# Performance work log

Measured on AMD Instinct MI355X. Metric: run time of the kernel, lower is better.

Reference implementation:

```python
import jax, jax.numpy as jnp
import numpy as np

B, T, H = 4096, 200, 64
NU, NI, NC = 100000, 1000000, 1000
AU_HID = 36
EPS = 1e-8


def dice(x, alpha):
    # Dice activation: p = sigmoid(batchnorm(x)); out = p*x + (1-p)*alpha*x
    axes = tuple(range(x.ndim - 1))
    m = jnp.mean(x, axis=axes, keepdims=True)
    v = jnp.var(x, axis=axes, keepdims=True)
    p = jax.nn.sigmoid((x - m) * jax.lax.rsqrt(v + EPS))
    return p * x + (1.0 - p) * alpha * x


def setup_inputs() -> dict:
    key = jax.random.key(0)
    ks = jax.random.split(key, 18)
    s = 0.02
    n = lambda k, shp: (jax.random.normal(k, shp, dtype=jnp.float32) * s)
    return {
        "user": jax.random.randint(ks[0], (B,), 0, NU),
        "hist": jax.random.randint(ks[1], (B, T), 0, NI),
        "item": jax.random.randint(ks[2], (B,), 0, NI),
        "cate": jax.random.randint(ks[3], (B,), 0, NC),
        "U": n(ks[4], (NU, H)),
        "I": n(ks[5], (NI, H)),
        "C": n(ks[6], (NC, H)),
        "au_W1": n(ks[7], (4 * H, AU_HID)),
        "au_b1": jnp.zeros((AU_HID,), jnp.float32),
        "au_a1": jnp.zeros((AU_HID,), jnp.float32),
        "au_W2": n(ks[8], (AU_HID, 1)),
        "au_b2": jnp.zeros((1,), jnp.float32),
        "W1": n(ks[9], (4 * H, 80)),
        "b1": jnp.zeros((80,), jnp.float32),
        "a1": jnp.zeros((80,), jnp.float32),
        "W2": n(ks[10], (80, 40)),
        "b2": jnp.zeros((40,), jnp.float32),
        "a2": jnp.zeros((40,), jnp.float32),
        "W3": n(ks[11], (40, 2)),
        "b3": jnp.zeros((2,), jnp.float32),
    }


def reference(user, hist, item, cate, U, I, C,
              au_W1, au_b1, au_a1, au_W2, au_b2,
              W1, b1, a1, W2, b2, a2, W3, b3):
    ue = U[user]            # [B,H]
    ie = I[item]            # [B,H]
    ce = C[cate]            # [B,H]
    he = I[hist]            # [B,T,H] history item embeddings (vectorized over the time loop)
    ieb = jnp.broadcast_to(ie[:, None, :], he.shape)
    # ActivationUnit: concat(hist, item, hist-item, hist*item) -> Linear -> Dice -> Linear(->1)
    au_in = jnp.concatenate([he, ieb, he - ieb, he * ieb], axis=-1)  # [B,T,4H]
    h1 = dice(au_in @ au_W1 + au_b1, au_a1)                          # [B,T,36]
    w = h1 @ au_W2 + au_b2                                           # [B,T,1]
    # weighted-sum pooling over history (original detaches via numpy round-trip)
    cur = jax.lax.stop_gradient(jnp.sum(w * he, axis=1))             # [B,H]
    x = jnp.concatenate([ue, ie, ce, cur], axis=-1)                  # [B,4H]
    x = dice(x @ W1 + b1, a1)
    x = dice(x @ W2 + b2, a2)
    return x @ W3 + b3                                               # [B,2]
```

## Files before the change

kernel.cpp:

```cpp
#include <hip/hip_runtime.h>
#include <math.h>

#define BB 4096
#define TT 200
#define NT (BB*TT)

typedef __attribute__((ext_vector_type(8))) __bf16 bf16x8;
typedef __attribute__((ext_vector_type(4))) float f32x4;
typedef __attribute__((ext_vector_type(4))) _Float16 f16x4;

static __device__ __forceinline__ unsigned short f2b(float f) {
  __bf16 b = (__bf16)f;
  return __builtin_bit_cast(unsigned short, b);
}

__global__ __launch_bounds__(256) void k_prep(
    const int* __restrict__ item, const float* __restrict__ Itab,
    const float* __restrict__ auW1, const float* __restrict__ auB1,
    const float* __restrict__ W1, float* __restrict__ TBuf,
    float* __restrict__ W1T) {
  const int blk = blockIdx.x, tid = threadIdx.x;
  if (blk >= BB) {
    int j = blk - BB;
    W1T[j * 256 + tid] = W1[tid * 80 + j];
    return;
  }
  __shared__ float sIe[64];
  if (tid < 64) sIe[tid] = Itab[(size_t)item[blk] * 64 + tid];
  __syncthreads();
  if (tid < 36) {
    const float* Wb_ = auW1 + 64 * 36;
    const float* Wc = auW1 + 128 * 36;
    float a = auB1[tid];
    for (int k = 0; k < 64; ++k)
      a += sIe[k] * (Wb_[k * 36 + tid] - Wc[k * 36 + tid]);
    TBuf[blk * 36 + tid] = a;
  }
}

__global__ __launch_bounds__(256, 3) void k_gemm1(
    const int* __restrict__ hist, const int* __restrict__ item,
    const float* __restrict__ Itab, const float* __restrict__ auW1,
    const float* __restrict__ TBuf, float* __restrict__ PART,
    _Float16* __restrict__ Xb) {
  const int b = blockIdx.x, tid = threadIdx.x;
  const int wv = tid >> 6, l = tid & 63;
  const int lr = l & 15, lq = l >> 4;
  __shared__ __align__(16) unsigned short sHe[208 * 72];
  __shared__ __align__(16) unsigned short sWBT[48 * 72];
  __shared__ float sR1[192], sR2[192];

  const float ie_reg = Itab[(size_t)item[b] * 64 + l];

  const int* hp = hist + b * TT;
  int rowi[13];
#pragma unroll
  for (int it = 0; it < 13; ++it) {
    int i = tid + it * 256;
    int ic = i < 3200 ? i : 3199;
    rowi[it] = hp[ic >> 4];
  }
  float4 v[13];
#pragma unroll
  for (int it = 0; it < 13; ++it) {
    int i = tid + it * 256;
    int ic = i < 3200 ? i : 3199;
    v[it] = ((const float4*)(Itab + (size_t)rowi[it] * 64))[ic & 15];
  }
#pragma unroll
  for (int it = 0; it < 13; ++it) {
    int i = tid + it * 256;
    if (i < 3200) {
      ushort4 u;
      u.x = f2b(v[it].x); u.y = f2b(v[it].y);
      u.z = f2b(v[it].z); u.w = f2b(v[it].w);
      *(ushort4*)(sHe + (i >> 4) * 72 + (i & 15) * 4) = u;
    }
  }
  for (int i = tid; i < 8 * 18; i += 256) {
    int r = TT + i / 18, c = i - (i / 18) * 18;
    *(ushort4*)(sHe + r * 72 + c * 4) = (ushort4){0, 0, 0, 0};
  }
  {
    const float* Wc = auW1 + 128 * 36;
    const float* Wd = auW1 + 192 * 36;
#pragma unroll
    for (int it = 0; it < 12; ++it) {
      int i = tid + it * 256;
      int k = i / 48, n = i - (i / 48) * 48;
      float w = 0.f;
      if (n < 36) {
        int idx = k * 36 + n;
        float iek = __shfl(ie_reg, k, 64);
        w = (auW1[idx] + Wc[idx]) + iek * Wd[idx];
      }
      sWBT[n * 72 + k] = f2b(w);
    }
  }
  float tb3[3];
#pragma unroll
  for (int nt = 0; nt < 3; ++nt) {
    int j = nt * 16 + lr;
    tb3[nt] = (j < 36) ? TBuf[b * 36 + j] : 0.f;
  }
  __syncthreads();

  bf16x8 bfr[3][2];
#pragma unroll
  for (int nt = 0; nt < 3; ++nt)
#pragma unroll
    for (int kh = 0; kh < 2; ++kh)
      bfr[nt][kh] = *reinterpret_cast<const bf16x8*>(
          sWBT + (nt * 16 + lr) * 72 + kh * 32 + lq * 8);

  f32x4 acc[4][3];
#pragma unroll
  for (int mi = 0; mi < 4; ++mi)
#pragma unroll
    for (int nt = 0; nt < 3; ++nt) acc[mi][nt] = (f32x4){0.f, 0.f, 0.f, 0.f};

#pragma unroll
  for (int mi = 0; mi < 4; ++mi) {
    const int mt = wv + mi * 4;
    if (mt <= 12) {
      const unsigned short* ap = sHe + (mt * 16 + lr) * 72 + lq * 8;
      bf16x8 a0 = *reinterpret_cast<const bf16x8*>(ap);
      bf16x8 a1 = *reinterpret_cast<const bf16x8*>(ap + 32);
#pragma unroll
      for (int nt = 0; nt < 3; ++nt) {
        acc[mi][nt] = __builtin_amdgcn_mfma_f32_16x16x32_bf16(
            a0, bfr[nt][0], acc[mi][nt], 0, 0, 0);
        acc[mi][nt] = __builtin_amdgcn_mfma_f32_16x16x32_bf16(
            a1, bfr[nt][1], acc[mi][nt], 0, 0, 0);
      }
    }
  }

  __syncthreads();
  _Float16* sXs = (_Float16*)sHe;

  float s1[3] = {0.f, 0.f, 0.f}, s2[3] = {0.f, 0.f, 0.f};
#pragma unroll
  for (int mi = 0; mi < 4; ++mi) {
    const int mt = wv + mi * 4;
    if (mt <= 12) {
#pragma unroll
      for (int q = 0; q < 4; ++q) {
        const int t = mt * 16 + lq * 4 + q;
        if (t < TT) {
#pragma unroll
          for (int nt = 0; nt < 3; ++nt) {
            const int j = nt * 16 + lr;
            float x = acc[mi][nt][q] + tb3[nt];
            if (j < 36) {
              s1[nt] += x;
              s2[nt] = fmaf(x, x, s2[nt]);
              sXs[t * 36 + j] = (_Float16)x;
            }
          }
        }
      }
    }
  }
#pragma unroll
  for (int nt = 0; nt < 3; ++nt) {
    float a = s1[nt], c = s2[nt];
    a += __shfl_xor(a, 16, 64); a += __shfl_xor(a, 32, 64);
    c += __shfl_xor(c, 16, 64); c += __shfl_xor(c, 32, 64);
    if (l < 16) {
      sR1[wv * 48 + nt * 16 + l] = a;
      sR2[wv * 48 + nt * 16 + l] = c;
    }
  }
  __syncthreads();
  if (tid < 36) {
    float a = sR1[tid] + sR1[48 + tid] + sR1[96 + tid] + sR1[144 + tid];
    float c = sR2[tid] + sR2[48 + tid] + sR2[96 + tid] + sR2[144 + tid];
    PART[b * 72 + tid] = a;
    PART[b * 72 + 36 + tid] = c;
  }
  {
    const uint4* src = (const uint4*)sXs;
    uint4* dst = (uint4*)(Xb + (size_t)b * 7200);
#pragma unroll
    for (int it = 0; it < 4; ++it) {
      int i = tid + it * 256;
      if (i < 900) dst[i] = src[i];
    }
  }
}

__global__ __launch_bounds__(256) void k_aust(const float* __restrict__ PART,
                                              float* __restrict__ AUST) {
  int ch = blockIdx.x, tid = threadIdx.x;
  float s1 = 0.f, s2 = 0.f;
  for (int blk = tid; blk < BB; blk += 256) {
    s1 += PART[blk * 72 + ch];
    s2 += PART[blk * 72 + 36 + ch];
  }
  __shared__ float r1[256], r2[256];
  r1[tid] = s1;
  r2[tid] = s2;
  __syncthreads();
  for (int off = 128; off > 0; off >>= 1) {
    if (tid < off) { r1[tid] += r1[tid + off]; r2[tid] += r2[tid + off]; }
    __syncthreads();
  }
  if (tid == 0) {
    float m = r1[0] / (float)NT;
    float var = r2[0] / (float)NT - m * m;
    AUST[ch] = m;
    AUST[36 + ch] = 1.0f / sqrtf(var + 1e-8f);
  }
}

__global__ __launch_bounds__(256) void k_att(
    const int* __restrict__ hist, const int* __restrict__ user,
    const int* __restrict__ item, const int* __restrict__ cate,
    const float* __restrict__ Itab, const float* __restrict__ Utab,
    const float* __restrict__ Ctab, const _Float16* __restrict__ Xb,
    const float* __restrict__ AUST, const float* __restrict__ auA1,
    const float* __restrict__ auW2, const float* __restrict__ auB2,
    const float* __restrict__ W1T, const float* __restrict__ b1,
    float* __restrict__ Y1) {
  const int b = blockIdx.x, tid = threadIdx.x;
  __shared__ float sW[TT];
  __shared__ int sRows[TT];
  __shared__ float sD[144];
  __shared__ float sPart[256];
  __shared__ float sX[256];
  if (tid < TT) sRows[tid] = hist[b * TT + tid];
  if (tid >= 208 && tid < 208 + 36) sD[tid - 208] = AUST[tid - 208];
  else if (tid < 36) sD[36 + tid] = AUST[36 + tid];
  else if (tid >= 64 && tid < 100) sD[72 + (tid - 64)] = auA1[tid - 64];
  else if (tid >= 128 && tid < 164) sD[108 + (tid - 128)] = auW2[tid - 128];
  __syncthreads();
  if (tid < TT) {
    const f16x4* xr = (const f16x4*)(Xb + (size_t)b * 7200 + tid * 36);
    float w = auB2[0];
#pragma unroll
    for (int p = 0; p < 9; ++p) {
      f16x4 pr = xr[p];
#pragma unroll
      for (int h = 0; h < 4; ++h) {
        int j = 4 * p + h;
        float x = (float)pr[h];
        float xh = (x - sD[j]) * sD[36 + j];
        float pp = 1.0f / (1.0f + __expf(-xh));
        float al = sD[72 + j];
        w = fmaf(x * (al + pp * (1.0f - al)), sD[108 + j], w);
      }
    }
    sW[tid] = w;
  }
  __syncthreads();
  {
    const int l = tid & 63, wv = tid >> 6;
    const int t0 = wv * 50;
    float c0 = 0.f, c1 = 0.f, c2 = 0.f, c3 = 0.f;
#pragma unroll
    for (int g = 0; g < 12; ++g) {
      int u = t0 + g * 4;
      c0 = fmaf(sW[u + 0], Itab[(size_t)sRows[u + 0] * 64 + l], c0);
      c1 = fmaf(sW[u + 1], Itab[(size_t)sRows[u + 1] * 64 + l], c1);
      c2 = fmaf(sW[u + 2], Itab[(size_t)sRows[u + 2] * 64 + l], c2);
      c3 = fmaf(sW[u + 3], Itab[(size_t)sRows[u + 3] * 64 + l], c3);
    }
    c0 = fmaf(sW[t0 + 48], Itab[(size_t)sRows[t0 + 48] * 64 + l], c0);
    c1 = fmaf(sW[t0 + 49], Itab[(size_t)sRows[t0 + 49] * 64 + l], c1);
    sPart[tid] = (c0 + c1) + (c2 + c3);
  }
  __syncthreads();
  if (tid < 64) {
    float cur = sPart[tid] + sPart[64 + tid] + sPart[128 + tid] + sPart[192 + tid];
    sX[tid] = Utab[(size_t)user[b] * 64 + tid];
    sX[64 + tid] = Itab[(size_t)item[b] * 64 + tid];
    sX[128 + tid] = Ctab[(size_t)cate[b] * 64 + tid];
    sX[192 + tid] = cur;
  }
  __syncthreads();
  if (tid < 80) {
    float a = b1[tid];
    const float4* wt = (const float4*)(W1T + tid * 256);
#pragma unroll 8
    for (int kq = 0; kq < 64; ++kq) {
      float4 w4 = wt[kq];
      a = fmaf(sX[kq * 4 + 0], w4.x, a);
      a = fmaf(sX[kq * 4 + 1], w4.y, a);
      a = fmaf(sX[kq * 4 + 2], w4.z, a);
      a = fmaf(sX[kq * 4 + 3], w4.w, a);
    }
    Y1[b * 80 + tid] = a;
  }
}

__global__ __launch_bounds__(256) void k_colstats(const float* __restrict__ src,
                                                  int nch, float* __restrict__ st) {
  int ch = blockIdx.x, tid = threadIdx.x;
  float s1 = 0.f, s2 = 0.f;
  for (int r = tid; r < BB; r += 256) {
    float v = src[r * nch + ch];
    s1 += v;
    s2 += v * v;
  }
  __shared__ float r1[256], r2[256];
  r1[tid] = s1;
  r2[tid] = s2;
  __syncthreads();
  for (int off = 128; off > 0; off >>= 1) {
    if (tid < off) { r1[tid] += r1[tid + off]; r2[tid] += r2[tid + off]; }
    __syncthreads();
  }
  if (tid == 0) {
    float m = r1[0] / (float)BB;
    float var = r2[0] / (float)BB - m * m;
    st[ch] = m;
    st[nch + ch] = 1.0f / sqrtf(var + 1e-8f);
  }
}

__global__ __launch_bounds__(128) void k_mlp2(const float* __restrict__ Y1,
                                              const float* __restrict__ ST80,
                                              const float* __restrict__ a1,
                                              const float* __restrict__ W2,
                                              const float* __restrict__ b2,
                                              float* __restrict__ Y2) {
  int b = blockIdx.x, tid = threadIdx.x;
  __shared__ float sY[80];
  if (tid < 80) {
    float x = Y1[b * 80 + tid];
    float xh = (x - ST80[tid]) * ST80[80 + tid];
    float p = 1.0f / (1.0f + expf(-xh));
    sY[tid] = p * x + (1.0f - p) * a1[tid] * x;
  }
  __syncthreads();
  if (tid < 40) {
    float a = b2[tid];
    for (int k = 0; k < 80; ++k) a += sY[k] * W2[k * 40 + tid];
    Y2[b * 40 + tid] = a;
  }
}

__global__ __launch_bounds__(64) void k_mlp3(const float* __restrict__ Y2,
                                             const float* __restrict__ ST40,
                                             const float* __restrict__ a2,
                                             const float* __restrict__ W3,
                                             const float* __restrict__ b3,
                                             float* __restrict__ out) {
  int b = blockIdx.x, tid = threadIdx.x;
  __shared__ float sY[40];
  if (tid < 40) {
    float x = Y2[b * 40 + tid];
    float xh = (x - ST40[tid]) * ST40[40 + tid];
    float p = 1.0f / (1.0f + expf(-xh));
    sY[tid] = p * x + (1.0f - p) * a2[tid] * x;
  }
  __syncthreads();
  if (tid < 2) {
    float a = b3[tid];
    for (int k = 0; k < 40; ++k) a += sY[k] * W3[k * 2 + tid];
    out[b * 2 + tid] = a;
  }
}

extern "C" void kernel_launch(void* const* d_in, const int* in_sizes, int n_in,
                              void* d_out, int out_size, void* d_ws, size_t ws_size,
                              hipStream_t stream) {
  const int* user = (const int*)d_in[0];
  const int* hist = (const int*)d_in[1];
  const int* item = (const int*)d_in[2];
  const int* cate = (const int*)d_in[3];
  const float* Utab = (const float*)d_in[4];
  const float* Itab = (const float*)d_in[5];
  const float* Ctab = (const float*)d_in[6];
  const float* auW1 = (const float*)d_in[7];
  const float* auB1 = (const float*)d_in[8];
  const float* auA1 = (const float*)d_in[9];
  const float* auW2 = (const float*)d_in[10];
  const float* auB2 = (const float*)d_in[11];
  const float* W1 = (const float*)d_in[12];
  const float* b1 = (const float*)d_in[13];
  const float* a1 = (const float*)d_in[14];
  const float* W2 = (const float*)d_in[15];
  const float* b2 = (const float*)d_in[16];
  const float* a2 = (const float*)d_in[17];
  const float* W3 = (const float*)d_in[18];
  const float* b3 = (const float*)d_in[19];
  float* out = (float*)d_out;

  float* ws = (float*)d_ws;
  float* TBuf = ws;
  float* PART = TBuf + BB * 36;
  float* AUST = PART + BB * 72;
  float* Y1 = AUST + 72;
  float* ST80 = Y1 + BB * 80;
  float* Y2 = ST80 + 160;
  float* ST40 = Y2 + BB * 40;
  float* W1T = ST40 + 80;
  _Float16* Xb = (_Float16*)(W1T + 80 * 256);

  k_prep<<<BB + 80, 256, 0, stream>>>(item, Itab, auW1, auB1, W1, TBuf, W1T);
  k_gemm1<<<BB, 256, 0, stream>>>(hist, item, Itab, auW1, TBuf, PART, Xb);
  k_aust<<<36, 256, 0, stream>>>(PART, AUST);
  k_att<<<BB, 256, 0, stream>>>(hist, user, item, cate, Itab, Utab, Ctab, Xb,
                                AUST, auA1, auW2, auB2, W1T, b1, Y1);
  k_colstats<<<80, 256, 0, stream>>>(Y1, 80, ST80);
  k_mlp2<<<BB, 128, 0, stream>>>(Y1, ST80, a1, W2, b2, Y2);
  k_colstats<<<40, 256, 0, stream>>>(Y2, 40, ST40);
  k_mlp3<<<BB, 64, 0, stream>>>(Y2, ST40, a2, W3, b3, out);
}
```

Before: 178.6 us.

## Split small dot products across more threads and raise gemm1 occupancy hint

Result: slower. 197.5 us (+10.6%).

```diff
diff --git a/kernel.cpp b/kernel.cpp
--- a/kernel.cpp
+++ b/kernel.cpp
@@ -26,19 +26,29 @@
     return;
   }
   __shared__ float sIe[64];
+  __shared__ float sP[36][8];
   if (tid < 64) sIe[tid] = Itab[(size_t)item[blk] * 64 + tid];
   __syncthreads();
-  if (tid < 36) {
+  if (tid < 252) {
+    int j = tid / 7, s = tid - (tid / 7) * 7;
     const float* Wb_ = auW1 + 64 * 36;
     const float* Wc = auW1 + 128 * 36;
+    int k0 = s * 10, k1 = (s == 6) ? 64 : (k0 + 10);
+    float a = 0.f;
+    for (int k = k0; k < k1; ++k)
+      a = fmaf(sIe[k], Wb_[k * 36 + j] - Wc[k * 36 + j], a);
+    sP[j][s] = a;
+  }
+  __syncthreads();
+  if (tid < 36) {
     float a = auB1[tid];
-    for (int k = 0; k < 64; ++k)
-      a += sIe[k] * (Wb_[k * 36 + tid] - Wc[k * 36 + tid]);
+#pragma unroll
+    for (int s = 0; s < 7; ++s) a += sP[tid][s];
     TBuf[blk * 36 + tid] = a;
   }
 }
 
-__global__ __launch_bounds__(256, 3) void k_gemm1(
+__global__ __launch_bounds__(256, 4) void k_gemm1(
     const int* __restrict__ hist, const int* __restrict__ item,
     const float* __restrict__ Itab, const float* __restrict__ auW1,
     const float* __restrict__ TBuf, float* __restrict__ PART,
@@ -229,6 +239,7 @@
   __shared__ float sD[144];
   __shared__ float sPart[256];
   __shared__ float sX[256];
+  __shared__ float sMp[160];
   if (tid < TT) sRows[tid] = hist[b * TT + tid];
   if (tid >= 208 && tid < 208 + 36) sD[tid - 208] = AUST[tid - 208];
   else if (tid < 36) sD[36 + tid] = AUST[36 + tid];
@@ -279,19 +290,24 @@
     sX[192 + tid] = cur;
   }
   __syncthreads();
-  if (tid < 80) {
-    float a = b1[tid];
-    const float4* wt = (const float4*)(W1T + tid * 256);
+  if (tid < 160) {
+    const int j = (tid < 80) ? tid : (tid - 80);
+    const int h = (tid < 80) ? 0 : 1;
+    const float4* wt = (const float4*)(W1T + j * 256 + h * 128);
+    const float* xs = sX + h * 128;
+    float a0 = 0.f, a1 = 0.f, a2 = 0.f, a3 = 0.f;
 #pragma unroll 8
-    for (int kq = 0; kq < 64; ++kq) {
+    for (int kq = 0; kq < 32; ++kq) {
       float4 w4 = wt[kq];
-      a = fmaf(sX[kq * 4 + 0], w4.x, a);
-      a = fmaf(sX[kq * 4 + 1], w4.y, a);
-      a = fmaf(sX[kq * 4 + 2], w4.z, a);
-      a = fmaf(sX[kq * 4 + 3], w4.w, a);
-    }
-    Y1[b * 80 + tid] = a;
-  }
+      a0 = fmaf(xs[kq * 4 + 0], w4.x, a0);
+      a1 = fmaf(xs[kq * 4 + 1], w4.y, a1);
+      a2 = fmaf(xs[kq * 4 + 2], w4.z, a2);
+      a3 = fmaf(xs[kq * 4 + 3], w4.w, a3);
+    }
+    sMp[h * 80 + j] = (a0 + a1) + (a2 + a3);
+  }
+  __syncthreads();
+  if (tid < 80) Y1[b * 80 + tid] = b1[tid] + sMp[tid] + sMp[80 + tid];
 }
 
 __global__ __launch_bounds__(256) void k_colstats(const float* __restrict__ src,
@@ -335,9 +351,12 @@
   }
   __syncthreads();
   if (tid < 40) {
-    float a = b2[tid];
-    for (int k = 0; k < 80; ++k) a += sY[k] * W2[k * 40 + tid];
-    Y2[b * 40 + tid] = a;
+    float a0 = b2[tid], a1_ = 0.f;
+    for (int k = 0; k < 80; k += 2) {
+      a0 = fmaf(sY[k], W2[k * 40 + tid], a0);
+      a1_ = fmaf(sY[k + 1], W2[(k + 1) * 40 + tid], a1_);
+    }
+    Y2[b * 40 + tid] = a0 + a1_;
   }
 }
 
@@ -357,9 +376,12 @@
   }
   __syncthreads();
   if (tid < 2) {
-    float a = b3[tid];
-    for (int k = 0; k < 40; ++k) a += sY[k] * W3[k * 2 + tid];
-    out[b * 2 + tid] = a;
+    float a0 = b3[tid], a1_ = 0.f;
+    for (int k = 0; k < 40; k += 2) {
+      a0 = fmaf(sY[k], W3[k * 2 + tid], a0);
+      a1_ = fmaf(sY[k + 1], W3[(k + 1) * 2 + tid], a1_);
+    }
+    out[b * 2 + tid] = a0 + a1_;
   }
 }
 
```
